# Kernel optimization log

Hardware: AMD Instinct MI355X
Metric: run time of the kernel (lower is better)

The kernel has to match this reference:

```python
import jax, jax.numpy as jnp
import numpy as np


def setup_inputs() -> dict:
    key = jax.random.key(0)
    ks = jax.random.split(key, 7)
    N, C_in, H, W = 32, 512, 56, 56
    C_sq, C_e1, C_e3 = 64, 256, 256
    return {
        "x": jax.random.normal(ks[0], (N, C_in, H, W), dtype=jnp.float32),
        "squeeze_w": jax.random.normal(ks[1], (C_sq, C_in), dtype=jnp.float32) * 0.05,
        "squeeze_b": jax.random.normal(ks[2], (C_sq,), dtype=jnp.float32) * 0.05,
        "expand1x1_w": jax.random.normal(ks[3], (C_e1, C_sq), dtype=jnp.float32) * 0.05,
        "expand1x1_b": jax.random.normal(ks[4], (C_e1,), dtype=jnp.float32) * 0.05,
        "expand3x3_w": jax.random.normal(ks[5], (C_e3, C_sq, 3, 3), dtype=jnp.float32) * 0.05,
        "expand3x3_b": jax.random.normal(ks[6], (C_e3,), dtype=jnp.float32) * 0.05,
    }


def reference(x, squeeze_w, squeeze_b, expand1x1_w, expand1x1_b, expand3x3_w, expand3x3_b):
    # Squeeze 1x1 conv + ReLU: [N,C_in,H,W] -> [N,C_sq,H,W]
    s = jax.nn.relu(
        jnp.einsum("oc,nchw->nohw", squeeze_w, x) + squeeze_b[None, :, None, None]
    )
    # Expand 1x1 branch + ReLU
    e1 = jax.nn.relu(
        jnp.einsum("oc,nchw->nohw", expand1x1_w, s) + expand1x1_b[None, :, None, None]
    )
    # Expand 3x3 branch (padding=1) + ReLU
    e3 = jax.lax.conv_general_dilated(
        s, expand3x3_w,
        window_strides=(1, 1), padding=((1, 1), (1, 1)),
        dimension_numbers=("NCHW", "OIHW", "NCHW"),
    )
    e3 = jax.nn.relu(e3 + expand3x3_b[None, :, None, None])
    # Channel concat: expand1x1 first, expand3x3 second
    return jnp.concatenate([e1, e3], axis=1)
```

## Files before the change

kernel.cpp:

```cpp
#include <hip/hip_runtime.h>
#include <cstdint>
#include <cstddef>


typedef _Float16 f16;
typedef __attribute__((ext_vector_type(8))) _Float16 f16x8;
typedef __attribute__((ext_vector_type(4))) _Float16 f16x4;
typedef __attribute__((ext_vector_type(4))) float    f32x4;

#define MFMA(a, b, c) __builtin_amdgcn_mfma_f32_16x16x32_f16((a), (b), (c), 0, 0, 0)

#define NIMG 32
#define CIN  512
#define HW   3136
#define W56  56
#define CSQ  64
#define CE   256

__global__ __launch_bounds__(256) void fire_prep(
    const float* __restrict__ sw, const float* __restrict__ e1w,
    const float* __restrict__ e3w,
    f16* __restrict__ Wsq, f16* __restrict__ W1, f16* __restrict__ W3)
{
    int t = blockIdx.x * 256 + threadIdx.x;
    if (t < CSQ * CIN) {
        Wsq[t] = (f16)sw[t];
    } else if (t < CSQ * CIN + CE * CSQ) {
        int j = t - CSQ * CIN;
        W1[j] = (f16)e1w[j];
    } else {
        int j = t - (CSQ * CIN + CE * CSQ);
        if (j < 9 * CE * CSQ) {
            int tap = j >> 14;
            int rem = j & 16383;
            int o = rem >> 6;
            int i = rem & 63;
            W3[j] = (f16)e3w[(o * CSQ + i) * 9 + tap];
        }
    }
}

__global__ __launch_bounds__(256) void fire_squeeze2(
    const float* __restrict__ x, const float* __restrict__ sb,
    const f16* __restrict__ Wsq, f16* __restrict__ Sws)
{
    const int tid  = threadIdx.x;
    const int lane = tid & 63, wv = tid >> 6;
    const int i = lane & 15, g = lane >> 4;
    const int w  = blockIdx.x * 4 + wv;
    const int n  = w / 49;
    const int p0 = (w % 49) * 64;

    const float* xp = x + (size_t)n * CIN * HW + p0 + 4 * i;

    f32x4 acc[4][4] = {};
    #pragma unroll
    for (int kk = 0; kk < 16; ++kk) {
        const int k0 = kk * 32 + g * 8;
        f16x8 b[4];
        #pragma unroll
        for (int v = 0; v < 8; ++v) {
            float4 q = *(const float4*)(xp + (size_t)(k0 + v) * HW);
            b[0][v] = (f16)q.x;
            b[1][v] = (f16)q.y;
            b[2][v] = (f16)q.z;
            b[3][v] = (f16)q.w;
        }
        #pragma unroll
        for (int m = 0; m < 4; ++m) {
            f16x8 a = *(const f16x8*)(Wsq + (16 * m + i) * CIN + k0);
            #pragma unroll
            for (int c = 0; c < 4; ++c)
                acc[m][c] = MFMA(a, b[c], acc[m][c]);
        }
    }

    #pragma unroll
    for (int m = 0; m < 4; ++m) {
        const int oc = 16 * m + 4 * g;
        const float4 bb = *(const float4*)(sb + oc);
        #pragma unroll
        for (int c = 0; c < 4; ++c) {
            const int px = p0 + 4 * i + c;
            f16x4 st;
            st[0] = (f16)fmaxf(acc[m][c][0] + bb.x, 0.f);
            st[1] = (f16)fmaxf(acc[m][c][1] + bb.y, 0.f);
            st[2] = (f16)fmaxf(acc[m][c][2] + bb.z, 0.f);
            st[3] = (f16)fmaxf(acc[m][c][3] + bb.w, 0.f);
            *(f16x4*)(Sws + ((size_t)n * HW + px) * CSQ + oc) = st;
        }
    }
}

__global__ __launch_bounds__(256) void fire_expand1(
    const f16* __restrict__ Sws, const f16* __restrict__ W1,
    const float* __restrict__ b1, float* __restrict__ out)
{
    const int tid  = threadIdx.x;
    const int lane = tid & 63, wv = tid >> 6;
    const int i = lane & 15, g = lane >> 4;
    const int n  = blockIdx.y;
    const int p0 = blockIdx.x * 64;

    f32x4 acc[4][4] = {};
    #pragma unroll
    for (int kk = 0; kk < 2; ++kk) {
        const int k0 = kk * 32 + g * 8;
        f16x8 b[4];
        #pragma unroll
        for (int c = 0; c < 4; ++c)
            b[c] = *(const f16x8*)(Sws + ((size_t)n * HW + p0 + 16 * c + i) * CSQ + k0);
        #pragma unroll
        for (int m = 0; m < 4; ++m) {
            f16x8 a = *(const f16x8*)(W1 + (64 * wv + 16 * m + i) * CSQ + k0);
            #pragma unroll
            for (int c = 0; c < 4; ++c)
                acc[m][c] = MFMA(a, b[c], acc[m][c]);
        }
    }

    #pragma unroll
    for (int m = 0; m < 4; ++m) {
        const int oc = 64 * wv + 16 * m + 4 * g;
        const float4 bb = *(const float4*)(b1 + oc);
        #pragma unroll
        for (int c = 0; c < 4; ++c) {
            float* op = out + ((size_t)n * 512 + oc) * HW + p0 + 16 * c + i;
            op[0 * (size_t)HW] = fmaxf(acc[m][c][0] + bb.x, 0.f);
            op[1 * (size_t)HW] = fmaxf(acc[m][c][1] + bb.y, 0.f);
            op[2 * (size_t)HW] = fmaxf(acc[m][c][2] + bb.z, 0.f);
            op[3 * (size_t)HW] = fmaxf(acc[m][c][3] + bb.w, 0.f);
        }
    }
}

__global__ __launch_bounds__(256) void fire_expand3(
    const f16* __restrict__ Sws, const f16* __restrict__ W3,
    const float* __restrict__ b3, float* __restrict__ out)
{
    __shared__ f16 Slds[4 * 58 * 64];

    const int tid  = threadIdx.x;
    const int lane = tid & 63, wv = tid >> 6;
    const int i = lane & 15, g = lane >> 4;
    const int n  = blockIdx.y;
    const int rb = blockIdx.x;
    const int r0 = rb * 2;

    #pragma unroll
    for (int it = 0; it < 8; ++it) {
        int task = it * 256 + tid;
        if (task < 232 * 8) {
            int s  = task >> 3, ck = task & 7;
            int tr = s / 58,   tc = s % 58;
            int h = r0 - 1 + tr, w = tc - 1;
            int4 val = make_int4(0, 0, 0, 0);
            if (h >= 0 && h < W56 && w >= 0 && w < W56)
                val = *(const int4*)(Sws + ((size_t)n * HW + h * W56 + w) * CSQ + ck * 8);
            int off = s * 128 + ck * 16;
            off ^= ((s & 7) << 4);
            *(int4*)((char*)Slds + off) = val;
        }
    }
    __syncthreads();

    int q0[7];
    #pragma unroll
    for (int c = 0; c < 7; ++c) {
        int pl  = 16 * c + i;
        int r   = (pl >= W56) ? 1 : 0;
        int col = pl - r * W56;
        q0[c] = r * 58 + col;
    }

    f32x4 acc[4][7] = {};
    for (int dh = 0; dh < 3; ++dh) {
        for (int dw = 0; dw < 3; ++dw) {
            const f16* wtap = W3 + (size_t)(dh * 3 + dw) * CE * CSQ;
            const int toff = dh * 58 + dw;
            #pragma unroll
            for (int kk = 0; kk < 2; ++kk) {
                const int k0 = kk * 32 + g * 8;
                f16x8 b[7];
                #pragma unroll
                for (int c = 0; c < 7; ++c) {
                    int q   = q0[c] + toff;
                    int off = q * 128 + kk * 64 + g * 16;
                    off ^= ((q & 7) << 4);
                    b[c] = *(const f16x8*)((const char*)Slds + off);
                }
                #pragma unroll
                for (int m = 0; m < 4; ++m) {
                    f16x8 a = *(const f16x8*)(wtap + (64 * wv + 16 * m + i) * CSQ + k0);
                    #pragma unroll
                    for (int c = 0; c < 7; ++c)
                        acc[m][c] = MFMA(a, b[c], acc[m][c]);
                }
            }
        }
    }

    #pragma unroll
    for (int m = 0; m < 4; ++m) {
        const int ocl = 64 * wv + 16 * m + 4 * g;
        const float4 bb = *(const float4*)(b3 + ocl);
        #pragma unroll
        for (int c = 0; c < 7; ++c) {
            float* op = out + ((size_t)n * 512 + 256 + ocl) * HW + rb * 112 + 16 * c + i;
            op[0 * (size_t)HW] = fmaxf(acc[m][c][0] + bb.x, 0.f);
            op[1 * (size_t)HW] = fmaxf(acc[m][c][1] + bb.y, 0.f);
            op[2 * (size_t)HW] = fmaxf(acc[m][c][2] + bb.z, 0.f);
            op[3 * (size_t)HW] = fmaxf(acc[m][c][3] + bb.w, 0.f);
        }
    }
}

extern "C" void kernel_launch(void* const* d_in, const int* in_sizes, int n_in,
                              void* d_out, int out_size, void* d_ws, size_t ws_size,
                              hipStream_t stream)
{
    const float* x  = (const float*)d_in[0];
    const float* sw = (const float*)d_in[1];
    const float* sb = (const float*)d_in[2];
    const float* w1 = (const float*)d_in[3];
    const float* b1 = (const float*)d_in[4];
    const float* w3 = (const float*)d_in[5];
    const float* b3 = (const float*)d_in[6];
    float* out = (float*)d_out;

    f16* Sws = (f16*)d_ws;
    f16* Wsq = Sws + (size_t)NIMG * HW * CSQ;
    f16* W1b = Wsq + CSQ * CIN;
    f16* W3b = W1b + CE * CSQ;

    fire_prep<<<768, 256, 0, stream>>>(sw, w1, w3, Wsq, W1b, W3b);
    fire_squeeze2<<<392, 256, 0, stream>>>(x, sb, Wsq, Sws);
    fire_expand1<<<dim3(49, 32), 256, 0, stream>>>(Sws, W1b, b1, out);
    fire_expand3<<<dim3(28, 32), 256, 0, stream>>>(Sws, W3b, b3, out);
}
```

Before: 175.1 us.

## Rewrite expand3x3 conv with 32x32x16 MFMA and 4-row by 32-col tiles

```diff
diff --git a/kernel.cpp b/kernel.cpp
--- a/kernel.cpp
+++ b/kernel.cpp
@@ -4,11 +4,13 @@
 
 
 typedef _Float16 f16;
-typedef __attribute__((ext_vector_type(8))) _Float16 f16x8;
-typedef __attribute__((ext_vector_type(4))) _Float16 f16x4;
-typedef __attribute__((ext_vector_type(4))) float    f32x4;
-
-#define MFMA(a, b, c) __builtin_amdgcn_mfma_f32_16x16x32_f16((a), (b), (c), 0, 0, 0)
+typedef __attribute__((ext_vector_type(8)))  _Float16 f16x8;
+typedef __attribute__((ext_vector_type(4)))  _Float16 f16x4;
+typedef __attribute__((ext_vector_type(4)))  float    f32x4;
+typedef __attribute__((ext_vector_type(16))) float    f32x16;
+
+#define MFMA(a, b, c)   __builtin_amdgcn_mfma_f32_16x16x32_f16((a), (b), (c), 0, 0, 0)
+#define MFMA32(a, b, c) __builtin_amdgcn_mfma_f32_32x32x16_f16((a), (b), (c), 0, 0, 0)
 
 #define NIMG 32
 #define CIN  512
@@ -30,12 +32,14 @@
         W1[j] = (f16)e1w[j];
     } else {
         int j = t - (CSQ * CIN + CE * CSQ);
-        if (j < 9 * CE * CSQ) {
+        if (j < 9 * 4 * 256 * 16) {
+            int v   = j & 7;
+            int h   = (j >> 3) & 1;
+            int o   = (j >> 4) & 255;
+            int kk  = (j >> 12) & 3;
             int tap = j >> 14;
-            int rem = j & 16383;
-            int o = rem >> 6;
-            int i = rem & 63;
-            W3[j] = (f16)e3w[(o * CSQ + i) * 9 + tap];
+            int ich = kk * 16 + h * 8 + v;
+            W3[j] = (f16)e3w[(o * CSQ + ich) * 9 + tap];
         }
     }
 }
@@ -134,83 +138,76 @@
     }
 }
 
-__global__ __launch_bounds__(256) void fire_expand3(
+__global__ __launch_bounds__(256) void fire_expand3v3(
     const f16* __restrict__ Sws, const f16* __restrict__ W3,
     const float* __restrict__ b3, float* __restrict__ out)
 {
-    __shared__ f16 Slds[4 * 58 * 64];
+    __shared__ f16 SK[8 * 204 * 8];
 
     const int tid  = threadIdx.x;
     const int lane = tid & 63, wv = tid >> 6;
-    const int i = lane & 15, g = lane >> 4;
+    const int l31 = lane & 31, h = lane >> 5;
+    const int wo = wv >> 1, wp = wv & 1;
+    const int rb = blockIdx.x >> 1, cb = blockIdx.x & 1;
     const int n  = blockIdx.y;
-    const int rb = blockIdx.x;
-    const int r0 = rb * 2;
-
-    #pragma unroll
-    for (int it = 0; it < 8; ++it) {
-        int task = it * 256 + tid;
-        if (task < 232 * 8) {
-            int s  = task >> 3, ck = task & 7;
-            int tr = s / 58,   tc = s % 58;
-            int h = r0 - 1 + tr, w = tc - 1;
+    const int r0 = rb * 4;
+
+    if (tid < 204) {
+        const int tr = tid / 34, tc = tid - tr * 34;
+        const int hi = r0 - 1 + tr;
+        const int wi = cb * 32 - 1 + tc;
+        const bool inb = (hi >= 0 && hi < W56 && wi >= 0 && wi < W56);
+        const f16* src = Sws + ((size_t)n * HW + hi * W56 + wi) * CSQ;
+        #pragma unroll
+        for (int ck = 0; ck < 8; ++ck) {
             int4 val = make_int4(0, 0, 0, 0);
-            if (h >= 0 && h < W56 && w >= 0 && w < W56)
-                val = *(const int4*)(Sws + ((size_t)n * HW + h * W56 + w) * CSQ + ck * 8);
-            int off = s * 128 + ck * 16;
-            off ^= ((s & 7) << 4);
-            *(int4*)((char*)Slds + off) = val;
+            if (inb) val = *(const int4*)(src + ck * 8);
+            *(int4*)((char*)SK + (ck * 204 + tid) * 16) = val;
         }
     }
     __syncthreads();
 
-    int q0[7];
-    #pragma unroll
-    for (int c = 0; c < 7; ++c) {
-        int pl  = 16 * c + i;
-        int r   = (pl >= W56) ? 1 : 0;
-        int col = pl - r * W56;
-        q0[c] = r * 58 + col;
-    }
-
-    f32x4 acc[4][7] = {};
-    for (int dh = 0; dh < 3; ++dh) {
-        for (int dw = 0; dw < 3; ++dw) {
-            const f16* wtap = W3 + (size_t)(dh * 3 + dw) * CE * CSQ;
-            const int toff = dh * 58 + dw;
-            #pragma unroll
-            for (int kk = 0; kk < 2; ++kk) {
-                const int k0 = kk * 32 + g * 8;
-                f16x8 b[7];
+    f32x16 acc[4][2] = {};
+
+    for (int tap = 0; tap < 9; ++tap) {
+        const int dh = tap / 3, dw = tap - dh * 3;
+        const int posb = (2 * wp + dh) * 34 + l31 + dw;
+        const f16* wbase = W3 + (size_t)tap * 4 * 256 * 16;
+        #pragma unroll
+        for (int kk = 0; kk < 4; ++kk) {
+            const char* kb = (const char*)SK + (kk * 2 + h) * 204 * 16;
+            f16x8 B0 = *(const f16x8*)(kb + posb * 16);
+            f16x8 B1 = *(const f16x8*)(kb + (posb + 34) * 16);
+            #pragma unroll
+            for (int om = 0; om < 4; ++om) {
+                f16x8 A = *(const f16x8*)(wbase + (size_t)kk * 256 * 16
+                                          + (wo * 128 + om * 32 + l31) * 16 + h * 8);
+                acc[om][0] = MFMA32(A, B0, acc[om][0]);
+                acc[om][1] = MFMA32(A, B1, acc[om][1]);
+            }
+        }
+    }
+
+    const int colg = cb * 32 + l31;
+    const bool ok = (colg < W56);
+    #pragma unroll
+    for (int om = 0; om < 4; ++om) {
+        const int ocb = wo * 128 + om * 32;
+        #pragma unroll
+        for (int c = 0; c < 2; ++c) {
+            const int row = r0 + 2 * wp + c;
+            float* obase = out + ((size_t)n * 512 + 256 + ocb) * HW + row * W56 + colg;
+            #pragma unroll
+            for (int q = 0; q < 4; ++q) {
+                const float4 bb = *(const float4*)(b3 + ocb + 8 * q + 4 * h);
+                const float bbv[4] = {bb.x, bb.y, bb.z, bb.w};
                 #pragma unroll
-                for (int c = 0; c < 7; ++c) {
-                    int q   = q0[c] + toff;
-                    int off = q * 128 + kk * 64 + g * 16;
-                    off ^= ((q & 7) << 4);
-                    b[c] = *(const f16x8*)((const char*)Slds + off);
-                }
-                #pragma unroll
-                for (int m = 0; m < 4; ++m) {
-                    f16x8 a = *(const f16x8*)(wtap + (64 * wv + 16 * m + i) * CSQ + k0);
-                    #pragma unroll
-                    for (int c = 0; c < 7; ++c)
-                        acc[m][c] = MFMA(a, b[c], acc[m][c]);
+                for (int rv = 0; rv < 4; ++rv) {
+                    const int ocl = 8 * q + 4 * h + rv;
+                    const float val = fmaxf(acc[om][c][q * 4 + rv] + bbv[rv], 0.f);
+                    if (ok) obase[(size_t)ocl * HW] = val;
                 }
             }
-        }
-    }
-
-    #pragma unroll
-    for (int m = 0; m < 4; ++m) {
-        const int ocl = 64 * wv + 16 * m + 4 * g;
-        const float4 bb = *(const float4*)(b3 + ocl);
-        #pragma unroll
-        for (int c = 0; c < 7; ++c) {
-            float* op = out + ((size_t)n * 512 + 256 + ocl) * HW + rb * 112 + 16 * c + i;
-            op[0 * (size_t)HW] = fmaxf(acc[m][c][0] + bb.x, 0.f);
-            op[1 * (size_t)HW] = fmaxf(acc[m][c][1] + bb.y, 0.f);
-            op[2 * (size_t)HW] = fmaxf(acc[m][c][2] + bb.z, 0.f);
-            op[3 * (size_t)HW] = fmaxf(acc[m][c][3] + bb.w, 0.f);
         }
     }
 }
@@ -236,5 +233,5 @@
     fire_prep<<<768, 256, 0, stream>>>(sw, w1, w3, Wsq, W1b, W3b);
     fire_squeeze2<<<392, 256, 0, stream>>>(x, sb, Wsq, Sws);
     fire_expand1<<<dim3(49, 32), 256, 0, stream>>>(Sws, W1b, b1, out);
-    fire_expand3<<<dim3(28, 32), 256, 0, stream>>>(Sws, W3b, b3, out);
-}
+    fire_expand3v3<<<dim3(28, 32), 256, 0, stream>>>(Sws, W3b, b3, out);
+}
```

After: 294.4 us. 68.1% more time.
